# Kernel tuning notes

Measured on AMD Instinct MI355X. Metric: run time of the kernel, lower is better.

Reference implementation:

```python
import jax, jax.numpy as jnp
import numpy as np
from jax import lax

B, S, D, G, V = 32, 8, 128, 32, 64   # batch, slots, hidden_dim, grid_size, vocab_size
K, ED = 128, 32                       # VQ codebook size, code dim


def _conv(x, w, b, pad):
    # standard Conv2d, NCHW / OIHW
    y = lax.conv_general_dilated(x, w, (1, 1), [(pad, pad), (pad, pad)],
                                 dimension_numbers=('NCHW', 'OIHW', 'NCHW'))
    return y + b[None, :, None, None]


def _convT(x, w, b):
    # ConvTranspose2d(k=5, stride=1, padding=2) == conv with spatially flipped
    # kernel, padding k-1-p = 2, channels swapped (IOHW layout of torch weight).
    y = lax.conv_general_dilated(x, jnp.flip(w, (2, 3)), (1, 1), [(2, 2), (2, 2)],
                                 dimension_numbers=('NCHW', 'IOHW', 'NCHW'))
    return y + b[None, :, None, None]


def _build_grid(h, w):
    ys = jnp.linspace(0.0, 1.0, h)
    xs = jnp.linspace(0.0, 1.0, w)
    gy, gx = jnp.meshgrid(ys, xs, indexing='ij')
    g = jnp.stack([gy, gx], axis=-1)                 # [H,W,2]
    return jnp.concatenate([g, 1.0 - g], axis=-1)    # [H,W,4]


def setup_inputs() -> dict:
    key = jax.random.key(0)
    ks = jax.random.split(key, 20)
    sc = 0.05
    n = lambda k, sh: jax.random.normal(k, sh, jnp.float32) * sc
    return {
        'latent': jax.random.normal(ks[0], (B, S, D), jnp.float32),
        'pos_w': n(ks[1], (D, 4)),            # Linear(4, hidden): [out,in]
        'pos_b': jnp.zeros((D,), jnp.float32),
        'ct1_w': n(ks[2], (D, 64, 5, 5)),     # ConvTranspose2d: [in,out,kH,kW]
        'ct1_b': jnp.zeros((64,), jnp.float32),
        'ct2_w': n(ks[3], (64, 32, 5, 5)),
        'ct2_b': jnp.zeros((32,), jnp.float32),
        'codebook': jax.random.uniform(ks[4], (K, ED), jnp.float32, -1.0 / K, 1.0 / K),
        'c1_w': n(ks[5], (64, 32, 3, 3)),     # Conv2d: [out,in,kH,kW]
        'c1_b': jnp.zeros((64,), jnp.float32),
        'c2_w': n(ks[6], (V, 64, 3, 3)),
        'c2_b': jnp.zeros((V,), jnp.float32),
        'a1_w': n(ks[7], (64, 32, 3, 3)),
        'a1_b': jnp.zeros((64,), jnp.float32),
        'a2_w': n(ks[8], (1, 64, 3, 3)),
        'a2_b': jnp.zeros((1,), jnp.float32),
    }


def _forward(latent, pos_w, pos_b, ct1_w, ct1_b, ct2_w, ct2_b, codebook,
             c1_w, c1_b, c2_w, c2_b, a1_w, a1_b, a2_w, a2_b):
    b, s, d = latent.shape
    # spatial broadcast of slot latents -> [B*S, D, H, W]
    z = jnp.broadcast_to(latent.reshape(b * s, d, 1, 1), (b * s, d, G, G))
    # soft position embedding
    grid = _build_grid(G, G)                                  # [H,W,4]
    pos = (grid @ pos_w.T + pos_b).transpose(2, 0, 1)[None]   # [1,D,H,W]
    z = z + pos
    # ConvTranspose decoder
    h = jax.nn.relu(_convT(z, ct1_w, ct1_b))
    feat = jax.nn.relu(_convT(h, ct2_w, ct2_b))               # [B*S,32,H,W]
    # VQ bottleneck on channel-last features
    fp = feat.transpose(0, 2, 3, 1)                           # [B*S,H,W,32]
    flat = fp.reshape(-1, ED)                                 # [N,32]
    dist = (jnp.sum(flat * flat, axis=1, keepdims=True)
            + jnp.sum(codebook * codebook, axis=1)
            - 2.0 * flat @ codebook.T)                        # [N,K]
    idx = jnp.argmin(dist, axis=1)                            # [N]
    q = codebook[idx].reshape(fp.shape)                       # gather lookup
    e_loss = jnp.mean((lax.stop_gradient(q) - fp) ** 2)
    q_loss = jnp.mean((q - lax.stop_gradient(fp)) ** 2)
    vq_loss = q_loss + 0.25 * e_loss
    q_ste = fp + lax.stop_gradient(q - fp)                    # straight-through
    vq_feat = q_ste.transpose(0, 3, 1, 2)                     # [B*S,32,H,W]
    # heads
    colors = _conv(jax.nn.silu(_conv(vq_feat, c1_w, c1_b, 1)), c2_w, c2_b, 1)
    colors = colors.reshape(b, s, V, G, G)
    alphas = _conv(jax.nn.silu(_conv(feat, a1_w, a1_b, 1)), a2_w, a2_b, 1)
    alphas = alphas.reshape(b, s, 1, G, G)
    alphas_n = jax.nn.softmax(alphas, axis=1)
    recon = jnp.sum(alphas_n * colors, axis=1)                # [B,V,H,W]
    return recon, alphas_n, vq_loss


def reference(latent, pos_w, pos_b, ct1_w, ct1_b, ct2_w, ct2_b, codebook,
              c1_w, c1_b, c2_w, c2_b, a1_w, a1_b, a2_w, a2_b):
    return _forward(latent, pos_w, pos_b, ct1_w, ct1_b, ct2_w, ct2_b, codebook,
                    c1_w, c1_b, c2_w, c2_b, a1_w, a1_b, a2_w, a2_b)
```

## Files before the change

### kernel.cpp

```cpp
#include <hip/hip_runtime.h>
#include <math.h>

#define AOFF 2097152
#define LOFF 2359296

typedef __attribute__((ext_vector_type(8))) short short8;
typedef __attribute__((ext_vector_type(4))) float f32x4;

__device__ __forceinline__ int clsf(int v) { return v < 2 ? v : (v > 29 ? v - 27 : 2); }

__device__ __forceinline__ unsigned int f2bfu(float x) {
    unsigned int u = __float_as_uint(x);
    return (u + 0x7FFFu + ((u >> 16) & 1u)) >> 16;
}
__device__ __forceinline__ unsigned int cvt2(float a, float b) {
    return f2bfu(a) | (f2bfu(b) << 16);
}
__device__ __forceinline__ float bf2f(unsigned short u) {
    return __uint_as_float(((unsigned int)u) << 16);
}

__global__ void w1t_kernel(const float* __restrict__ w1, float* __restrict__ w1t) {
    int idx = blockIdx.x * 256 + threadIdx.x;
    if (idx >= 204800) return;
    int tap = idx % 25, rest = idx / 25;
    w1t[tap * 8192 + rest] = w1[idx];
}

__global__ void tapabc_kernel(const float* __restrict__ pw, const float* __restrict__ pb,
                              const float* __restrict__ w1t, float* __restrict__ tapabc) {
    __shared__ float A3[384];
    int tap = blockIdx.x, t = threadIdx.x;
    if (t < 128) {
        float p0 = pw[t * 4], p1 = pw[t * 4 + 1], p2 = pw[t * 4 + 2], p3 = pw[t * 4 + 3];
        A3[t] = p2 + p3 + pb[t];
        A3[128 + t] = p0 - p2;
        A3[256 + t] = p1 - p3;
    }
    __syncthreads();
    int o = t & 63, comp = t >> 6;
    const float* wp = w1t + tap * 8192 + o;
    const float* a = A3 + comp * 128;
    float s = 0.f;
    for (int i = 0; i < 128; ++i) s = fmaf(wp[i * 64], a[i], s);
    tapabc[(tap * 64 + o) * 3 + comp] = s;
}

__global__ void pfill_kernel(const float* __restrict__ tapabc, const float* __restrict__ b1,
                             float* __restrict__ P2) {
    __shared__ float uv[75];
    int o = blockIdx.x, t = threadIdx.x;
    if (t < 75) {
        int cls = t / 3, comp = t % 3;
        int cy = cls / 5, cx = cls % 5;
        const int klo[5] = {2, 1, 0, 0, 0}, khi[5] = {4, 4, 4, 3, 2};
        const float inv31 = 1.f / 31.f;
        float s = (comp == 0) ? b1[o] : 0.f;
        for (int ky = klo[cy]; ky <= khi[cy]; ++ky)
            for (int kx = klo[cx]; kx <= khi[cx]; ++kx) {
                int tap = (4 - ky) * 5 + (4 - kx);
                const float* tp = &tapabc[(tap * 64 + o) * 3];
                if (comp == 0) s += tp[0] + tp[1] * (ky - 2) * inv31 + tp[2] * (kx - 2) * inv31;
                else if (comp == 1) s += tp[1] * inv31;
                else s += tp[2] * inv31;
            }
        uv[t] = s;
    }
    __syncthreads();
    int y = t >> 5, x = t & 31;
    int cls = clsf(y) * 5 + clsf(x);
    float val = uv[cls * 3] + uv[cls * 3 + 1] * y + uv[cls * 3 + 2] * x;
    P2[((o >> 1) << 11) + (t << 1) + (o & 1)] = val;
}

__global__ void wsum_kernel(const float* __restrict__ w1, float* __restrict__ Wsum) {
    int idx = blockIdx.x * 256 + threadIdx.x;
    if (idx >= 25 * 128 * 64) return;
    int cls = idx >> 13;
    int i = (idx >> 6) & 127;
    int o = idx & 63;
    int cy = cls / 5, cx = cls % 5;
    const int klo[5] = {2, 1, 0, 0, 0}, khi[5] = {4, 4, 4, 3, 2};
    float s = 0.f;
    for (int ky = klo[cy]; ky <= khi[cy]; ++ky)
        for (int kx = klo[cx]; kx <= khi[cx]; ++kx)
            s += w1[(i * 64 + o) * 25 + (4 - ky) * 5 + (4 - kx)];
    Wsum[idx] = s;
}

__global__ void m_kernel(const float* __restrict__ latent, const float* __restrict__ Wsum,
                         float* __restrict__ M) {
    int n = blockIdx.x, cls = blockIdx.y, o = threadIdx.x;
    const float* l = &latent[n * 128];
    const float* w = &Wsum[cls * 8192 + o];
    float a0 = 0.f, a1 = 0.f;
    for (int i = 0; i < 128; i += 2) {
        a0 = fmaf(l[i], w[i * 64], a0);
        a1 = fmaf(l[i + 1], w[(i + 1) * 64], a1);
    }
    M[(n * 25 + cls) * 64 + o] = a0 + a1;
}

__global__ void prep_all_kernel(const float* __restrict__ a1w, const float* __restrict__ c1w,
                                const float* __restrict__ c2w, const float* __restrict__ ct2w,
                                short* __restrict__ wtall) {
    int gid = blockIdx.x * 256 + threadIdx.x;
    if (gid < 36864) {
        const float* src = gid < 18432 ? a1w : c1w;
        int idx = gid < 18432 ? gid : gid - 18432;
        int j = idx & 7, fi = idx >> 3;
        int o = fi % 64, g = (fi / 64) & 3, t = fi / 256;
        int i = g * 8 + j;
        wtall[gid] = (short)f2bfu(src[(o * 32 + i) * 9 + (t / 3) * 3 + (t % 3)]);
    } else if (gid < 73728) {
        int idx = gid - 36864;
        int j = idx & 7, fi = idx >> 3;
        int o = fi % 64, g = (fi / 64) & 3, ks = (fi / 256) & 1, t = fi / 512;
        int i = ks * 32 + g * 8 + j;
        wtall[gid] = (short)f2bfu(c2w[(o * 64 + i) * 9 + (t / 3) * 3 + (t % 3)]);
    } else if (gid < 124928) {
        int idx = gid - 73728;
        int j = idx & 7, fi = idx >> 3;
        int o = fi & 31, g = (fi >> 5) & 3, ks = (fi >> 7) & 1, t = fi >> 8;
        int i = ks * 32 + g * 8 + j;
        int ky = t / 5, kx = t % 5;
        wtall[gid] = (short)f2bfu(ct2w[((i * 32 + o) * 5 + (4 - ky)) * 5 + (4 - kx)]);
    }
}

__global__ __launch_bounds__(256) void conv5_kernel(
        const float* __restrict__ M, const float* __restrict__ P2,
        const short* __restrict__ wt, const float* __restrict__ b2,
        unsigned short* __restrict__ featb) {
    __shared__ __align__(16) short tile[12 * 36 * 40];
    __shared__ float Ml[1600];
    const int n = blockIdx.x, y0 = blockIdx.y * 8;
    const int tid = threadIdx.x, w = tid >> 6, l = tid & 63;
    const int lx = l & 15, lg = l >> 4;

    for (int e = tid; e < 1600; e += 256) Ml[e] = M[n * 1600 + e];
    __syncthreads();

    f32x4 acc[2][2][2];
    #pragma unroll
    for (int m = 0; m < 2; ++m)
        #pragma unroll
        for (int q = 0; q < 2; ++q)
            #pragma unroll
            for (int c = 0; c < 2; ++c) acc[m][q][c] = (f32x4){0.f, 0.f, 0.f, 0.f};

    #pragma unroll 1
    for (int ks = 0; ks < 2; ++ks) {
        if (ks) __syncthreads();
        for (int e = tid; e < 6912; e += 256) {
            int cx = e % 36;
            int q = e / 36;
            int ipl = q & 15;
            int r = q >> 4;
            int gy = y0 - 2 + r, gx = cx - 2;
            unsigned int pack = 0u;
            if (gy >= 0 && gy < 32 && gx >= 0 && gx < 32) {
                int cls = clsf(gy) * 5 + clsf(gx);
                int pp = gy * 32 + gx;
                float2 pv = ((const float2*)P2)[((ks * 16 + ipl) << 10) + pp];
                float2 ml = ((const float2*)Ml)[cls * 32 + ks * 16 + ipl];
                pack = cvt2(fmaxf(ml.x + pv.x, 0.f), fmaxf(ml.y + pv.y, 0.f));
            }
            *(unsigned int*)((char*)tile + (r * 36 + cx) * 80 + ipl * 4) = pack;
        }
        __syncthreads();
        for (int kx = 0; kx < 5; ++kx) {
            short8 af[5][2];
            #pragma unroll
            for (int ky = 0; ky < 5; ++ky)
                #pragma unroll
                for (int m = 0; m < 2; ++m)
                    af[ky][m] = *(const short8*)(wt + (ky * 5 + kx) * 2048 +
                                                 ((ks * 4 + lg) * 32 + m * 16 + lx) * 8);
            #pragma unroll
            for (int colf = 0; colf < 2; ++colf) {
                const int cbase = ((2 * w) * 36 + kx + colf * 16 + lx) * 80 + lg * 16;
                short8 bc[6];
                #pragma unroll
                for (int ir = 0; ir < 6; ++ir)
                    bc[ir] = *(const short8*)((char*)tile + cbase + ir * (36 * 80));
                #pragma unroll
                for (int ky = 0; ky < 5; ++ky)
                    #pragma unroll
                    for (int q = 0; q < 2; ++q)
                        #pragma unroll
                        for (int m = 0; m < 2; ++m)
                            acc[m][q][colf] = __builtin_amdgcn_mfma_f32_16x16x32_bf16(
                                af[ky][m], bc[q + ky], acc[m][q][colf], 0, 0, 0);
            }
        }
    }

    #pragma unroll
    for (int m = 0; m < 2; ++m)
        #pragma unroll
        for (int q = 0; q < 2; ++q)
            #pragma unroll
            for (int colf = 0; colf < 2; ++colf) {
                int yl = 2 * w + q, x = colf * 16 + lx;
                unsigned long long pk = 0ull;
                #pragma unroll
                for (int r = 0; r < 4; ++r) {
                    int och = m * 16 + lg * 4 + r;
                    float v = fmaxf(acc[m][q][colf][r] + b2[och], 0.f);
                    pk |= (unsigned long long)f2bfu(v) << (16 * r);
                }
                *(unsigned long long*)(featb + (n * 1024 + (y0 + yl) * 32 + x) * 32
                                       + m * 16 + lg * 4) = pk;
            }
}

__device__ __forceinline__ void conv3_core(
        const short* __restrict__ tile, const short* __restrict__ wt, int abase,
        f32x4 (&acc)[4][2][2], int w, int lx, int lg) {
    #pragma unroll
    for (int kx = 0; kx < 3; ++kx) {
        short8 af[3][4];
        #pragma unroll
        for (int ky = 0; ky < 3; ++ky)
            #pragma unroll
            for (int m = 0; m < 4; ++m)
                af[ky][m] = *(const short8*)(wt + (ky * 3 + kx) * abase +
                                             (lg * 64 + m * 16 + lx) * 8);
        #pragma unroll
        for (int colf = 0; colf < 2; ++colf) {
            const int cbase = ((2 * w) * 34 + kx + colf * 16 + lx) * 80 + lg * 16;
            short8 bc[4];
            #pragma unroll
            for (int ir = 0; ir < 4; ++ir)
                bc[ir] = *(const short8*)((const char*)tile + cbase + ir * (34 * 80));
            #pragma unroll
            for (int ky = 0; ky < 3; ++ky)
                #pragma unroll
                for (int q = 0; q < 2; ++q)
                    #pragma unroll
                    for (int m = 0; m < 4; ++m)
                        acc[m][q][colf] = __builtin_amdgcn_mfma_f32_16x16x32_bf16(
                            af[ky][m], bc[q + ky], acc[m][q][colf], 0, 0, 0);
        }
    }
}

__device__ __forceinline__ void conv3_epi(
        f32x4 (&acc)[4][2][2], const float* __restrict__ bias,
        unsigned short* __restrict__ out_, int n, int y0, int w, int lx, int lg, int act) {
    #pragma unroll
    for (int m = 0; m < 4; ++m)
        #pragma unroll
        for (int q = 0; q < 2; ++q)
            #pragma unroll
            for (int colf = 0; colf < 2; ++colf) {
                int yl = 2 * w + q, x = colf * 16 + lx;
                unsigned long long pk = 0ull;
                #pragma unroll
                for (int r = 0; r < 4; ++r) {
                    int och = m * 16 + lg * 4 + r;
                    float v = acc[m][q][colf][r] + bias[och];
                    if (act) v = v / (1.f + expf(-v));
                    pk |= (unsigned long long)f2bfu(v) << (16 * r);
                }
                *(unsigned long long*)(out_ + (n * 1024 + (y0 + yl) * 32 + x) * 64
                                       + m * 16 + lg * 4) = pk;
            }
}

template<int ACT>
__global__ __launch_bounds__(256) void conv3d_kernel(
        const unsigned short* __restrict__ in_, const short* __restrict__ wt,
        const float* __restrict__ bias, unsigned short* __restrict__ out_) {
    __shared__ __align__(16) short tileA[10 * 34 * 40];
    __shared__ __align__(16) short tileB[10 * 34 * 40];
    const int n0 = blockIdx.x * 2, y0 = blockIdx.y * 8;
    const int tid = threadIdx.x, w = tid >> 6, l = tid & 63;
    const int lx = l & 15, lg = l >> 4;

    short8 rA[6], rB[6];
    int pxv[6], qcv[6];
    #pragma unroll
    for (int it = 0; it < 6; ++it) {
        int e = tid + it * 256;
        short8 v8 = (short8){0, 0, 0, 0, 0, 0, 0, 0};
        int px = e >> 2, qc = e & 3;
        pxv[it] = px; qcv[it] = qc;
        if (e < 1360) {
            int r = px / 34, cx = px - r * 34;
            int gy = y0 - 1 + r, gx = cx - 1;
            if (gy >= 0 && gy < 32 && gx >= 0 && gx < 32)
                v8 = *(const short8*)(in_ + (n0 * 1024 + gy * 32 + gx) * 32 + qc * 8);
        }
        rA[it] = v8;
    }
    #pragma unroll
    for (int it = 0; it < 6; ++it)
        if (tid + it * 256 < 1360)
            *(short8*)((char*)tileA + pxv[it] * 80 + qcv[it] * 16) = rA[it];
    #pragma unroll
    for (int it = 0; it < 6; ++it) {
        int e = tid + it * 256;
        short8 v8 = (short8){0, 0, 0, 0, 0, 0, 0, 0};
        if (e < 1360) {
            int px = pxv[it], qc = qcv[it];
            int r = px / 34, cx = px - r * 34;
            int gy = y0 - 1 + r, gx = cx - 1;
            if (gy >= 0 && gy < 32 && gx >= 0 && gx < 32)
                v8 = *(const short8*)(in_ + ((n0 + 1) * 1024 + gy * 32 + gx) * 32 + qc * 8);
        }
        rB[it] = v8;
    }
    __syncthreads();

    f32x4 acc[4][2][2];
    #pragma unroll
    for (int m = 0; m < 4; ++m)
        #pragma unroll
        for (int q = 0; q < 2; ++q)
            #pragma unroll
            for (int c = 0; c < 2; ++c) acc[m][q][c] = (f32x4){0.f, 0.f, 0.f, 0.f};
    conv3_core(tileA, wt, 2048, acc, w, lx, lg);

    #pragma unroll
    for (int it = 0; it < 6; ++it)
        if (tid + it * 256 < 1360)
            *(short8*)((char*)tileB + pxv[it] * 80 + qcv[it] * 16) = rB[it];
    conv3_epi(acc, bias, out_, n0, y0, w, lx, lg, ACT);
    __syncthreads();

    #pragma unroll
    for (int m = 0; m < 4; ++m)
        #pragma unroll
        for (int q = 0; q < 2; ++q)
            #pragma unroll
            for (int c = 0; c < 2; ++c) acc[m][q][c] = (f32x4){0.f, 0.f, 0.f, 0.f};
    conv3_core(tileB, wt, 2048, acc, w, lx, lg);
    conv3_epi(acc, bias, out_, n0 + 1, y0, w, lx, lg, ACT);
}

__global__ __launch_bounds__(256) void c2_kernel(
        const unsigned short* __restrict__ in_, const short* __restrict__ wt,
        const float* __restrict__ bias, unsigned short* __restrict__ out_) {
    __shared__ __align__(16) short smem[10 * 34 * 40];
    const int n = blockIdx.x, y0 = blockIdx.y * 8;
    const int tid = threadIdx.x, w = tid >> 6, l = tid & 63;
    const int lx = l & 15, lg = l >> 4;

    short8 r0[6], r1[6];
    int pxv[6], qcv[6];
    #pragma unroll
    for (int it = 0; it < 6; ++it) {
        int e = tid + it * 256;
        int px = e >> 2, qc = e & 3;
        pxv[it] = px; qcv[it] = qc;
        short8 v0 = (short8){0, 0, 0, 0, 0, 0, 0, 0};
        short8 v1 = v0;
        if (e < 1360) {
            int r = px / 34, cx = px - r * 34;
            int gy = y0 - 1 + r, gx = cx - 1;
            if (gy >= 0 && gy < 32 && gx >= 0 && gx < 32) {
                const unsigned short* p = in_ + (n * 1024 + gy * 32 + gx) * 64 + qc * 8;
                v0 = *(const short8*)p;
                v1 = *(const short8*)(p + 32);
            }
        }
        r0[it] = v0; r1[it] = v1;
    }
    #pragma unroll
    for (int it = 0; it < 6; ++it)
        if (tid + it * 256 < 1360)
            *(short8*)((char*)smem + pxv[it] * 80 + qcv[it] * 16) = r0[it];
    __syncthreads();

    f32x4 acc[4][2][2];
    #pragma unroll
    for (int m = 0; m < 4; ++m)
        #pragma unroll
        for (int q = 0; q < 2; ++q)
            #pragma unroll
            for (int c = 0; c < 2; ++c) acc[m][q][c] = (f32x4){0.f, 0.f, 0.f, 0.f};

    #pragma unroll
    for (int kx = 0; kx < 3; ++kx) {
        short8 af[3][4];
        #pragma unroll
        for (int ky = 0; ky < 3; ++ky)
            #pragma unroll
            for (int m = 0; m < 4; ++m)
                af[ky][m] = *(const short8*)(wt + (ky * 3 + kx) * 4096 +
                                             ((0 * 4 + lg) * 64 + m * 16 + lx) * 8);
        #pragma unroll
        for (int colf = 0; colf < 2; ++colf) {
            const int cbase = ((2 * w) * 34 + kx + colf * 16 + lx) * 80 + lg * 16;
            short8 bc[4];
            #pragma unroll
            for (int ir = 0; ir < 4; ++ir)
                bc[ir] = *(const short8*)((char*)smem + cbase + ir * (34 * 80));
            #pragma unroll
            for (int ky = 0; ky < 3; ++ky)
                #pragma unroll
                for (int q = 0; q < 2; ++q)
                    #pragma unroll
                    for (int m = 0; m < 4; ++m)
                        acc[m][q][colf] = __builtin_amdgcn_mfma_f32_16x16x32_bf16(
                            af[ky][m], bc[q + ky], acc[m][q][colf], 0, 0, 0);
        }
    }
    __syncthreads();
    #pragma unroll
    for (int it = 0; it < 6; ++it)
        if (tid + it * 256 < 1360)
            *(short8*)((char*)smem + pxv[it] * 80 + qcv[it] * 16) = r1[it];
    __syncthreads();
    #pragma unroll
    for (int kx = 0; kx < 3; ++kx) {
        short8 af[3][4];
        #pragma unroll
        for (int ky = 0; ky < 3; ++ky)
            #pragma unroll
            for (int m = 0; m < 4; ++m)
                af[ky][m] = *(const short8*)(wt + (ky * 3 + kx) * 4096 +
                                             ((1 * 4 + lg) * 64 + m * 16 + lx) * 8);
        #pragma unroll
        for (int colf = 0; colf < 2; ++colf) {
            const int cbase = ((2 * w) * 34 + kx + colf * 16 + lx) * 80 + lg * 16;
            short8 bc[4];
            #pragma unroll
            for (int ir = 0; ir < 4; ++ir)
                bc[ir] = *(const short8*)((char*)smem + cbase + ir * (34 * 80));
            #pragma unroll
            for (int ky = 0; ky < 3; ++ky)
                #pragma unroll
                for (int q = 0; q < 2; ++q)
                    #pragma unroll
                    for (int m = 0; m < 4; ++m)
                        acc[m][q][colf] = __builtin_amdgcn_mfma_f32_16x16x32_bf16(
                            af[ky][m], bc[q + ky], acc[m][q][colf], 0, 0, 0);
        }
    }

    #pragma unroll
    for (int m = 0; m < 4; ++m)
        #pragma unroll
        for (int q = 0; q < 2; ++q)
            #pragma unroll
            for (int colf = 0; colf < 2; ++colf) {
                int yl = 2 * w + q, x = colf * 16 + lx;
                unsigned long long pk = 0ull;
                #pragma unroll
                for (int r = 0; r < 4; ++r) {
                    int och = m * 16 + lg * 4 + r;
                    float v = acc[m][q][colf][r] + bias[och];
                    pk |= (unsigned long long)f2bfu(v) << (16 * r);
                }
                *(unsigned long long*)(out_ + (n * 1024 + (y0 + yl) * 32 + x) * 64
                                       + m * 16 + lg * 4) = pk;
            }
}

__global__ void a2dot_kernel(const unsigned short* __restrict__ in, const float* __restrict__ w,
                             float* __restrict__ s9) {
    __shared__ float wl[576];
    int t = threadIdx.x;
    for (int e = t; e < 576; e += 256) wl[e] = w[e];
    __syncthreads();
    int p = blockIdx.x * 256 + t;
    float acc[9];
    #pragma unroll
    for (int k = 0; k < 9; ++k) acc[k] = 0.f;
    const unsigned short* ip = in + (long long)p * 64;
    #pragma unroll
    for (int c8 = 0; c8 < 8; ++c8) {
        short8 v8 = *(const short8*)(ip + c8 * 8);
        #pragma unroll
        for (int j = 0; j < 8; ++j) {
            float v = bf2f((unsigned short)v8[j]);
            #pragma unroll
            for (int k = 0; k < 9; ++k) acc[k] = fmaf(v, wl[(c8 * 8 + j) * 9 + k], acc[k]);
        }
    }
    #pragma unroll
    for (int k = 0; k < 9; ++k) s9[(k << 18) + p] = acc[k];
}

__global__ void a2soft_kernel(const float* __restrict__ s9, const float* __restrict__ b2,
                              float* __restrict__ outp) {
    int idx = blockIdx.x * 256 + threadIdx.x;
    if (idx >= 32 * 1024) return;
    int bb = idx >> 10, yx = idx & 1023;
    int y = yx >> 5, x = yx & 31;
    float v[8];
    float bias = b2[0];
    #pragma unroll
    for (int s = 0; s < 8; ++s) {
        int n = bb * 8 + s;
        float a = bias;
        #pragma unroll
        for (int ky = 0; ky < 3; ++ky) {
            int yy = y + ky - 1;
            if (yy < 0 || yy > 31) continue;
            #pragma unroll
            for (int kx = 0; kx < 3; ++kx) {
                int xx = x + kx - 1;
                if (xx < 0 || xx > 31) continue;
                a += s9[((ky * 3 + kx) << 18) + (n << 10) + yy * 32 + xx];
            }
        }
        v[s] = a;
    }
    float m = -3.4e38f;
    #pragma unroll
    for (int s = 0; s < 8; ++s) m = fmaxf(m, v[s]);
    float sum = 0.f;
    #pragma unroll
    for (int s = 0; s < 8; ++s) { v[s] = expf(v[s] - m); sum += v[s]; }
    float inv = 1.f / sum;
    #pragma unroll
    for (int s = 0; s < 8; ++s) outp[AOFF + ((bb * 8 + s) << 10) + yx] = v[s] * inv;
}

__global__ __launch_bounds__(256) void vq_mfma_kernel(
        const unsigned short* __restrict__ featb, const float* __restrict__ codebook,
        unsigned short* __restrict__ qfeat, float* __restrict__ partial) {
    __shared__ float cbf[4096];
    __shared__ __align__(16) short cbh[4096];
    __shared__ float cn[128];
    __shared__ float red[4];
    const int tid = threadIdx.x;
    const int w = tid >> 6, l = tid & 63;
    const int lx = l & 15, lg = l >> 4;

    for (int e = tid; e < 4096; e += 256) {
        float v = codebook[e];
        cbf[e] = v;
        int code = e >> 5, d = e & 31;
        int off = (code * 32 + d) * 2;
        off ^= (code & 7) << 4;
        *(short*)((char*)cbh + off) = (short)f2bfu(v);
    }
    __syncthreads();
    if (tid < 128) {
        float s = 0.f;
        #pragma unroll
        for (int c = 0; c < 32; ++c) { float v = cbf[tid * 32 + c]; s = fmaf(v, v, s); }
        cn[tid] = s;
    }
    short8 af[8];
    #pragma unroll
    for (int m = 0; m < 8; ++m) {
        int code = m * 16 + lx;
        int off = (code * 32 + lg * 8) * 2;
        off ^= (code & 7) << 4;
        af[m] = *(const short8*)((char*)cbh + off);
    }
    __syncthreads();
    float cnh[8][4];
    #pragma unroll
    for (int m = 0; m < 8; ++m)
        #pragma unroll
        for (int r = 0; r < 4; ++r)
            cnh[m][r] = 0.5f * cn[m * 16 + lg * 4 + r];

    const int n = blockIdx.x >> 2;
    const int yxw = (blockIdx.x & 3) * 256 + w * 64;
    float lloss = 0.f;

    #pragma unroll 1
    for (int pxg = 0; pxg < 4; ++pxg) {
        int yx = yxw + pxg * 16 + lx;
        short8 bbs = *(const short8*)(featb + (n * 1024 + yx) * 32 + lg * 8);
        f32x4 S[8];
        #pragma unroll
        for (int m = 0; m < 8; ++m)
            S[m] = __builtin_amdgcn_mfma_f32_16x16x32_bf16(
                af[m], bbs, (f32x4){0.f, 0.f, 0.f, 0.f}, 0, 0, 0);
        float bestv = -3.4e38f; int besti = 0;
        #pragma unroll
        for (int m = 0; m < 8; ++m)
            #pragma unroll
            for (int r = 0; r < 4; ++r) {
                float v = S[m][r] - cnh[m][r];
                int code = m * 16 + lg * 4 + r;
                if (v > bestv) { bestv = v; besti = code; }
            }
        #pragma unroll
        for (int d = 16; d < 64; d <<= 1) {
            float ov = __shfl_xor(bestv, d);
            int oi = __shfl_xor(besti, d);
            if (ov > bestv || (ov == bestv && oi < besti)) { bestv = ov; besti = oi; }
        }
        int offq = (besti * 32 + lg * 8) * 2;
        offq ^= (besti & 7) << 4;
        short8 qh = *(const short8*)((char*)cbh + offq);
        *(short8*)(qfeat + (n * 1024 + yx) * 32 + lg * 8) = qh;
        const float* qf = &cbf[besti * 32 + lg * 8];
        #pragma unroll
        for (int j = 0; j < 8; ++j) {
            float fv = bf2f((unsigned short)bbs[j]);
            float dd = qf[j] - fv;
            lloss = fmaf(dd, dd, lloss);
        }
    }
    for (int off = 32; off > 0; off >>= 1) lloss += __shfl_down(lloss, off);
    if (l == 0) red[w] = lloss;
    __syncthreads();
    if (tid == 0) partial[blockIdx.x] = (red[0] + red[1]) + (red[2] + red[3]);
}

__global__ __launch_bounds__(256) void recon_kernel(
        const unsigned short* __restrict__ colors, float* __restrict__ outp) {
    const int b = blockIdx.x, y8 = blockIdx.y;
    const int tid = threadIdx.x;
    const int yxl = tid & 127, vh = tid >> 7;
    const int yx = y8 * 128 + yxl;
    float acc[32];
    #pragma unroll
    for (int v = 0; v < 32; ++v) acc[v] = 0.f;
    #pragma unroll 1
    for (int s = 0; s < 8; ++s) {
        float a = outp[AOFF + ((b * 8 + s) << 10) + yx];
        const unsigned short* cp = colors + ((b * 8 + s) * 1024 + yx) * 64 + vh * 32;
        #pragma unroll
        for (int k = 0; k < 4; ++k) {
            short8 v8 = *(const short8*)(cp + k * 8);
            #pragma unroll
            for (int j = 0; j < 8; ++j)
                acc[k * 8 + j] = fmaf(a, bf2f((unsigned short)v8[j]), acc[k * 8 + j]);
        }
    }
    #pragma unroll
    for (int v = 0; v < 32; ++v)
        outp[(b * 64 + vh * 32 + v) * 1024 + yx] = acc[v];
}

__global__ void loss_kernel(const float* __restrict__ partial, float* __restrict__ outp) {
    __shared__ float red[4];
    int t = threadIdx.x;
    float s = 0.f;
    for (int i = t; i < 1024; i += 256) s += partial[i];
    for (int o = 32; o > 0; o >>= 1) s += __shfl_down(s, o);
    if ((t & 63) == 0) red[t >> 6] = s;
    __syncthreads();
    if (t == 0) outp[LOFF] = 1.25f * ((red[0] + red[1]) + (red[2] + red[3])) / 8388608.0f;
}

extern "C" void kernel_launch(void* const* d_in, const int* in_sizes, int n_in,
                              void* d_out, int out_size, void* d_ws, size_t ws_size,
                              hipStream_t stream) {
    const float* latent  = (const float*)d_in[0];
    const float* pos_w   = (const float*)d_in[1];
    const float* pos_b   = (const float*)d_in[2];
    const float* ct1_w   = (const float*)d_in[3];
    const float* ct1_b   = (const float*)d_in[4];
    const float* ct2_w   = (const float*)d_in[5];
    const float* ct2_b   = (const float*)d_in[6];
    const float* codebook= (const float*)d_in[7];
    const float* c1_w    = (const float*)d_in[8];
    const float* c1_b    = (const float*)d_in[9];
    const float* c2_w    = (const float*)d_in[10];
    const float* c2_b    = (const float*)d_in[11];
    const float* a1_w    = (const float*)d_in[12];
    const float* a1_b    = (const float*)d_in[13];
    const float* a2_w    = (const float*)d_in[14];
    const float* a2_b    = (const float*)d_in[15];
    float* out = (float*)d_out;

    float* ws     = (float*)d_ws;
    unsigned short* featb = (unsigned short*)ws;
    float* s9     = ws + 8388608;
    float* tapabc = s9 + 2359296;
    float* P      = tapabc + 4800;
    float* M      = P + 65536;
    float* partial= M + 409600;
    float* w1t    = partial + 1024;
    float* Wsum   = w1t + 204800;
    short* wtall  = (short*)(Wsum + 204800);
    short* wtA    = wtall;
    short* wtC1   = wtall + 18432;
    short* wtC2   = wtall + 36864;
    short* wtT2   = wtall + 73728;
    unsigned short* tmpb    = (unsigned short*)(wtall + 124928);
    unsigned short* qfeatb  = tmpb + 16777216;
    unsigned short* colorsb = qfeatb + 8388608;

    w1t_kernel<<<800, 256, 0, stream>>>(ct1_w, w1t);
    tapabc_kernel<<<25, 192, 0, stream>>>(pos_w, pos_b, w1t, tapabc);
    pfill_kernel<<<64, 1024, 0, stream>>>(tapabc, ct1_b, P);
    wsum_kernel<<<800, 256, 0, stream>>>(ct1_w, Wsum);
    m_kernel<<<dim3(256, 25), 64, 0, stream>>>(latent, Wsum, M);
    prep_all_kernel<<<488, 256, 0, stream>>>(a1_w, c1_w, c2_w, ct2_w, wtall);

    conv5_kernel<<<dim3(256, 4), 256, 0, stream>>>(M, P, wtT2, ct2_b, featb);
    conv3d_kernel<1><<<dim3(128, 4), 256, 0, stream>>>(featb, wtA, a1_b, tmpb);
    a2dot_kernel<<<1024, 256, 0, stream>>>(tmpb, a2_w, s9);
    a2soft_kernel<<<128, 256, 0, stream>>>(s9, a2_b, out);
    vq_mfma_kernel<<<1024, 256, 0, stream>>>(featb, codebook, qfeatb, partial);
    conv3d_kernel<1><<<dim3(128, 4), 256, 0, stream>>>(qfeatb, wtC1, c1_b, tmpb);
    c2_kernel<<<dim3(256, 4), 256, 0, stream>>>(tmpb, wtC2, c2_b, colorsb);
    recon_kernel<<<dim3(32, 8), 256, 0, stream>>>(colorsb, out);
    loss_kernel<<<1, 256, 0, stream>>>(partial, out);
}
```

Measured before the change: 218.0 us.

## Merge independent head stages into heterogeneous kernels sharing one grid

Independent stages now share launches through a blockIdx.y split. The a1 conv and VQ quantization run together in one kernel, and the c1 conv and a2 dot product in a second; the old one-image-at-a-time conv3 replaces the two-image double-buffered tile pipeline. This is meant to cut launch count and fill the GPU better by overlapping unrelated work. The cost is lost overlap of the second image's load with compute, uneven block durations within one grid, and the colors buffer now aliasing the a1 output scratch.

```diff
diff --git a/kernel.cpp b/kernel.cpp
--- a/kernel.cpp
+++ b/kernel.cpp
@@ -215,9 +215,29 @@
             }
 }
 
-__device__ __forceinline__ void conv3_core(
-        const short* __restrict__ tile, const short* __restrict__ wt, int abase,
-        f32x4 (&acc)[4][2][2], int w, int lx, int lg) {
+__device__ __forceinline__ void conv3_img(
+        const unsigned short* __restrict__ in_, const short* __restrict__ wt,
+        const float* __restrict__ bias, unsigned short* __restrict__ out_,
+        short* __restrict__ smem, int n, int y0, int tid, int act) {
+    const int w = tid >> 6, l = tid & 63;
+    const int lx = l & 15, lg = l >> 4;
+    for (int e = tid; e < 1360; e += 256) {
+        int px = e >> 2, qc = e & 3;
+        int r = px / 34, cx = px - r * 34;
+        int gy = y0 - 1 + r, gx = cx - 1;
+        short8 v8 = (short8){0, 0, 0, 0, 0, 0, 0, 0};
+        if (gy >= 0 && gy < 32 && gx >= 0 && gx < 32)
+            v8 = *(const short8*)(in_ + (n * 1024 + gy * 32 + gx) * 32 + qc * 8);
+        *(short8*)((char*)smem + px * 80 + qc * 16) = v8;
+    }
+    __syncthreads();
+    f32x4 acc[4][2][2];
+    #pragma unroll
+    for (int m = 0; m < 4; ++m)
+        #pragma unroll
+        for (int q = 0; q < 2; ++q)
+            #pragma unroll
+            for (int c = 0; c < 2; ++c) acc[m][q][c] = (f32x4){0.f, 0.f, 0.f, 0.f};
     #pragma unroll
     for (int kx = 0; kx < 3; ++kx) {
         short8 af[3][4];
@@ -225,7 +245,7 @@
         for (int ky = 0; ky < 3; ++ky)
             #pragma unroll
             for (int m = 0; m < 4; ++m)
-                af[ky][m] = *(const short8*)(wt + (ky * 3 + kx) * abase +
+                af[ky][m] = *(const short8*)(wt + (ky * 3 + kx) * 2048 +
                                              (lg * 64 + m * 16 + lx) * 8);
         #pragma unroll
         for (int colf = 0; colf < 2; ++colf) {
@@ -233,7 +253,7 @@
             short8 bc[4];
             #pragma unroll
             for (int ir = 0; ir < 4; ++ir)
-                bc[ir] = *(const short8*)((const char*)tile + cbase + ir * (34 * 80));
+                bc[ir] = *(const short8*)((const char*)smem + cbase + ir * (34 * 80));
             #pragma unroll
             for (int ky = 0; ky < 3; ++ky)
                 #pragma unroll
@@ -244,11 +264,6 @@
                             af[ky][m], bc[q + ky], acc[m][q][colf], 0, 0, 0);
         }
     }
-}
-
-__device__ __forceinline__ void conv3_epi(
-        f32x4 (&acc)[4][2][2], const float* __restrict__ bias,
-        unsigned short* __restrict__ out_, int n, int y0, int w, int lx, int lg, int act) {
     #pragma unroll
     for (int m = 0; m < 4; ++m)
         #pragma unroll
@@ -269,75 +284,132 @@
             }
 }
 
-template<int ACT>
-__global__ __launch_bounds__(256) void conv3d_kernel(
-        const unsigned short* __restrict__ in_, const short* __restrict__ wt,
-        const float* __restrict__ bias, unsigned short* __restrict__ out_) {
-    __shared__ __align__(16) short tileA[10 * 34 * 40];
-    __shared__ __align__(16) short tileB[10 * 34 * 40];
-    const int n0 = blockIdx.x * 2, y0 = blockIdx.y * 8;
-    const int tid = threadIdx.x, w = tid >> 6, l = tid & 63;
+__global__ __launch_bounds__(256) void head1_kernel(
+        const unsigned short* __restrict__ featb, const float* __restrict__ codebook,
+        const short* __restrict__ wtA, const float* __restrict__ a1b,
+        unsigned short* __restrict__ a1out, unsigned short* __restrict__ qfeat,
+        float* __restrict__ partial) {
+    __shared__ __align__(16) char smraw[27648];
+    const int tid = threadIdx.x, n = blockIdx.x;
+    if (blockIdx.y < 4) {
+        conv3_img(featb, wtA, a1b, a1out, (short*)smraw, n, blockIdx.y * 8, tid, 1);
+        return;
+    }
+    float* cbf = (float*)smraw;
+    short* cbh = (short*)(smraw + 16384);
+    float* cn  = (float*)(smraw + 24576);
+    float* red = (float*)(smraw + 25088);
+    const int w = tid >> 6, l = tid & 63;
     const int lx = l & 15, lg = l >> 4;
 
-    short8 rA[6], rB[6];
-    int pxv[6], qcv[6];
-    #pragma unroll
-    for (int it = 0; it < 6; ++it) {
-        int e = tid + it * 256;
-        short8 v8 = (short8){0, 0, 0, 0, 0, 0, 0, 0};
-        int px = e >> 2, qc = e & 3;
-        pxv[it] = px; qcv[it] = qc;
-        if (e < 1360) {
-            int r = px / 34, cx = px - r * 34;
-            int gy = y0 - 1 + r, gx = cx - 1;
-            if (gy >= 0 && gy < 32 && gx >= 0 && gx < 32)
-                v8 = *(const short8*)(in_ + (n0 * 1024 + gy * 32 + gx) * 32 + qc * 8);
-        }
-        rA[it] = v8;
-    }
-    #pragma unroll
-    for (int it = 0; it < 6; ++it)
-        if (tid + it * 256 < 1360)
-            *(short8*)((char*)tileA + pxv[it] * 80 + qcv[it] * 16) = rA[it];
-    #pragma unroll
-    for (int it = 0; it < 6; ++it) {
-        int e = tid + it * 256;
-        short8 v8 = (short8){0, 0, 0, 0, 0, 0, 0, 0};
-        if (e < 1360) {
-            int px = pxv[it], qc = qcv[it];
-            int r = px / 34, cx = px - r * 34;
-            int gy = y0 - 1 + r, gx = cx - 1;
-            if (gy >= 0 && gy < 32 && gx >= 0 && gx < 32)
-                v8 = *(const short8*)(in_ + ((n0 + 1) * 1024 + gy * 32 + gx) * 32 + qc * 8);
-        }
-        rB[it] = v8;
-    }
-    __syncthreads();
-
-    f32x4 acc[4][2][2];
-    #pragma unroll
-    for (int m = 0; m < 4; ++m)
-        #pragma unroll
-        for (int q = 0; q < 2; ++q)
-            #pragma unroll
-            for (int c = 0; c < 2; ++c) acc[m][q][c] = (f32x4){0.f, 0.f, 0.f, 0.f};
-    conv3_core(tileA, wt, 2048, acc, w, lx, lg);
-
-    #pragma unroll
-    for (int it = 0; it < 6; ++it)
-        if (tid + it * 256 < 1360)
-            *(short8*)((char*)tileB + pxv[it] * 80 + qcv[it] * 16) = rB[it];
-    conv3_epi(acc, bias, out_, n0, y0, w, lx, lg, ACT);
-    __syncthreads();
-
-    #pragma unroll
-    for (int m = 0; m < 4; ++m)
-        #pragma unroll
-        for (int q = 0; q < 2; ++q)
-            #pragma unroll
-            for (int c = 0; c < 2; ++c) acc[m][q][c] = (f32x4){0.f, 0.f, 0.f, 0.f};
-    conv3_core(tileB, wt, 2048, acc, w, lx, lg);
-    conv3_epi(acc, bias, out_, n0 + 1, y0, w, lx, lg, ACT);
+    for (int e = tid; e < 4096; e += 256) {
+        float v = codebook[e];
+        cbf[e] = v;
+        int code = e >> 5, d = e & 31;
+        int off = (code * 32 + d) * 2;
+        off ^= (code & 7) << 4;
+        *(short*)((char*)cbh + off) = (short)f2bfu(v);
+    }
+    __syncthreads();
+    if (tid < 128) {
+        float s = 0.f;
+        #pragma unroll
+        for (int c = 0; c < 32; ++c) { float v = cbf[tid * 32 + c]; s = fmaf(v, v, s); }
+        cn[tid] = s;
+    }
+    short8 af[8];
+    #pragma unroll
+    for (int m = 0; m < 8; ++m) {
+        int code = m * 16 + lx;
+        int off = (code * 32 + lg * 8) * 2;
+        off ^= (code & 7) << 4;
+        af[m] = *(const short8*)((char*)cbh + off);
+    }
+    __syncthreads();
+    float cnh[8][4];
+    #pragma unroll
+    for (int m = 0; m < 8; ++m)
+        #pragma unroll
+        for (int r = 0; r < 4; ++r)
+            cnh[m][r] = 0.5f * cn[m * 16 + lg * 4 + r];
+
+    float lloss = 0.f;
+    #pragma unroll 1
+    for (int it = 0; it < 16; ++it) {
+        int yx = w * 256 + (it >> 2) * 64 + (it & 3) * 16 + lx;
+        short8 bbs = *(const short8*)(featb + (n * 1024 + yx) * 32 + lg * 8);
+        f32x4 S[8];
+        #pragma unroll
+        for (int m = 0; m < 8; ++m)
+            S[m] = __builtin_amdgcn_mfma_f32_16x16x32_bf16(
+                af[m], bbs, (f32x4){0.f, 0.f, 0.f, 0.f}, 0, 0, 0);
+        float bestv = -3.4e38f; int besti = 0;
+        #pragma unroll
+        for (int m = 0; m < 8; ++m)
+            #pragma unroll
+            for (int r = 0; r < 4; ++r) {
+                float v = S[m][r] - cnh[m][r];
+                int code = m * 16 + lg * 4 + r;
+                if (v > bestv) { bestv = v; besti = code; }
+            }
+        #pragma unroll
+        for (int d = 16; d < 64; d <<= 1) {
+            float ov = __shfl_xor(bestv, d);
+            int oi = __shfl_xor(besti, d);
+            if (ov > bestv || (ov == bestv && oi < besti)) { bestv = ov; besti = oi; }
+        }
+        int offq = (besti * 32 + lg * 8) * 2;
+        offq ^= (besti & 7) << 4;
+        short8 qh = *(const short8*)((char*)cbh + offq);
+        *(short8*)(qfeat + (n * 1024 + yx) * 32 + lg * 8) = qh;
+        const float* qf = &cbf[besti * 32 + lg * 8];
+        #pragma unroll
+        for (int j = 0; j < 8; ++j) {
+            float fv = bf2f((unsigned short)bbs[j]);
+            float dd = qf[j] - fv;
+            lloss = fmaf(dd, dd, lloss);
+        }
+    }
+    for (int off = 32; off > 0; off >>= 1) lloss += __shfl_down(lloss, off);
+    if (l == 0) red[w] = lloss;
+    __syncthreads();
+    if (tid == 0) partial[n] = (red[0] + red[1]) + (red[2] + red[3]);
+}
+
+__global__ __launch_bounds__(256) void head2_kernel(
+        const unsigned short* __restrict__ qfeat, const short* __restrict__ wtC1,
+        const float* __restrict__ c1b, unsigned short* __restrict__ c1out,
+        const unsigned short* __restrict__ a1out, const float* __restrict__ a2w,
+        float* __restrict__ s9) {
+    __shared__ __align__(16) char smraw[27648];
+    const int tid = threadIdx.x, n = blockIdx.x;
+    if (blockIdx.y < 4) {
+        conv3_img(qfeat, wtC1, c1b, c1out, (short*)smraw, n, blockIdx.y * 8, tid, 1);
+        return;
+    }
+    float* wl = (float*)smraw;
+    for (int e = tid; e < 576; e += 256) wl[e] = a2w[e];
+    __syncthreads();
+    #pragma unroll 1
+    for (int pp = 0; pp < 4; ++pp) {
+        int p = (n << 10) + pp * 256 + tid;
+        float acc[9];
+        #pragma unroll
+        for (int k = 0; k < 9; ++k) acc[k] = 0.f;
+        const unsigned short* ip = a1out + (long long)p * 64;
+        #pragma unroll
+        for (int c8 = 0; c8 < 8; ++c8) {
+            short8 v8 = *(const short8*)(ip + c8 * 8);
+            #pragma unroll
+            for (int j = 0; j < 8; ++j) {
+                float v = bf2f((unsigned short)v8[j]);
+                #pragma unroll
+                for (int k = 0; k < 9; ++k) acc[k] = fmaf(v, wl[(c8 * 8 + j) * 9 + k], acc[k]);
+            }
+        }
+        #pragma unroll
+        for (int k = 0; k < 9; ++k) s9[(k << 18) + p] = acc[k];
+    }
 }
 
 __global__ __launch_bounds__(256) void c2_kernel(
@@ -390,7 +462,7 @@
             #pragma unroll
             for (int m = 0; m < 4; ++m)
                 af[ky][m] = *(const short8*)(wt + (ky * 3 + kx) * 4096 +
-                                             ((0 * 4 + lg) * 64 + m * 16 + lx) * 8);
+                                             (lg * 64 + m * 16 + lx) * 8);
         #pragma unroll
         for (int colf = 0; colf < 2; ++colf) {
             const int cbase = ((2 * w) * 34 + kx + colf * 16 + lx) * 80 + lg * 16;
@@ -422,7 +494,7 @@
             #pragma unroll
             for (int m = 0; m < 4; ++m)
                 af[ky][m] = *(const short8*)(wt + (ky * 3 + kx) * 4096 +
-                                             ((1 * 4 + lg) * 64 + m * 16 + lx) * 8);
+                                             ((4 + lg) * 64 + m * 16 + lx) * 8);
         #pragma unroll
         for (int colf = 0; colf < 2; ++colf) {
             const int cbase = ((2 * w) * 34 + kx + colf * 16 + lx) * 80 + lg * 16;
@@ -458,31 +530,6 @@
                 *(unsigned long long*)(out_ + (n * 1024 + (y0 + yl) * 32 + x) * 64
                                        + m * 16 + lg * 4) = pk;
             }
-}
-
-__global__ void a2dot_kernel(const unsigned short* __restrict__ in, const float* __restrict__ w,
-                             float* __restrict__ s9) {
-    __shared__ float wl[576];
-    int t = threadIdx.x;
-    for (int e = t; e < 576; e += 256) wl[e] = w[e];
-    __syncthreads();
-    int p = blockIdx.x * 256 + t;
-    float acc[9];
-    #pragma unroll
-    for (int k = 0; k < 9; ++k) acc[k] = 0.f;
-    const unsigned short* ip = in + (long long)p * 64;
-    #pragma unroll
-    for (int c8 = 0; c8 < 8; ++c8) {
-        short8 v8 = *(const short8*)(ip + c8 * 8);
-        #pragma unroll
-        for (int j = 0; j < 8; ++j) {
-            float v = bf2f((unsigned short)v8[j]);
-            #pragma unroll
-            for (int k = 0; k < 9; ++k) acc[k] = fmaf(v, wl[(c8 * 8 + j) * 9 + k], acc[k]);
-        }
-    }
-    #pragma unroll
-    for (int k = 0; k < 9; ++k) s9[(k << 18) + p] = acc[k];
 }
 
 __global__ void a2soft_kernel(const float* __restrict__ s9, const float* __restrict__ b2,
@@ -521,94 +568,6 @@
     for (int s = 0; s < 8; ++s) outp[AOFF + ((bb * 8 + s) << 10) + yx] = v[s] * inv;
 }
 
-__global__ __launch_bounds__(256) void vq_mfma_kernel(
-        const unsigned short* __restrict__ featb, const float* __restrict__ codebook,
-        unsigned short* __restrict__ qfeat, float* __restrict__ partial) {
-    __shared__ float cbf[4096];
-    __shared__ __align__(16) short cbh[4096];
-    __shared__ float cn[128];
-    __shared__ float red[4];
-    const int tid = threadIdx.x;
-    const int w = tid >> 6, l = tid & 63;
-    const int lx = l & 15, lg = l >> 4;
-
-    for (int e = tid; e < 4096; e += 256) {
-        float v = codebook[e];
-        cbf[e] = v;
-        int code = e >> 5, d = e & 31;
-        int off = (code * 32 + d) * 2;
-        off ^= (code & 7) << 4;
-        *(short*)((char*)cbh + off) = (short)f2bfu(v);
-    }
-    __syncthreads();
-    if (tid < 128) {
-        float s = 0.f;
-        #pragma unroll
-        for (int c = 0; c < 32; ++c) { float v = cbf[tid * 32 + c]; s = fmaf(v, v, s); }
-        cn[tid] = s;
-    }
-    short8 af[8];
-    #pragma unroll
-    for (int m = 0; m < 8; ++m) {
-        int code = m * 16 + lx;
-        int off = (code * 32 + lg * 8) * 2;
-        off ^= (code & 7) << 4;
-        af[m] = *(const short8*)((char*)cbh + off);
-    }
-    __syncthreads();
-    float cnh[8][4];
-    #pragma unroll
-    for (int m = 0; m < 8; ++m)
-        #pragma unroll
-        for (int r = 0; r < 4; ++r)
-            cnh[m][r] = 0.5f * cn[m * 16 + lg * 4 + r];
-
-    const int n = blockIdx.x >> 2;
-    const int yxw = (blockIdx.x & 3) * 256 + w * 64;
-    float lloss = 0.f;
-
-    #pragma unroll 1
-    for (int pxg = 0; pxg < 4; ++pxg) {
-        int yx = yxw + pxg * 16 + lx;
-        short8 bbs = *(const short8*)(featb + (n * 1024 + yx) * 32 + lg * 8);
-        f32x4 S[8];
-        #pragma unroll
-        for (int m = 0; m < 8; ++m)
-            S[m] = __builtin_amdgcn_mfma_f32_16x16x32_bf16(
-                af[m], bbs, (f32x4){0.f, 0.f, 0.f, 0.f}, 0, 0, 0);
-        float bestv = -3.4e38f; int besti = 0;
-        #pragma unroll
-        for (int m = 0; m < 8; ++m)
-            #pragma unroll
-            for (int r = 0; r < 4; ++r) {
-                float v = S[m][r] - cnh[m][r];
-                int code = m * 16 + lg * 4 + r;
-                if (v > bestv) { bestv = v; besti = code; }
-            }
-        #pragma unroll
-        for (int d = 16; d < 64; d <<= 1) {
-            float ov = __shfl_xor(bestv, d);
-            int oi = __shfl_xor(besti, d);
-            if (ov > bestv || (ov == bestv && oi < besti)) { bestv = ov; besti = oi; }
-        }
-        int offq = (besti * 32 + lg * 8) * 2;
-        offq ^= (besti & 7) << 4;
-        short8 qh = *(const short8*)((char*)cbh + offq);
-        *(short8*)(qfeat + (n * 1024 + yx) * 32 + lg * 8) = qh;
-        const float* qf = &cbf[besti * 32 + lg * 8];
-        #pragma unroll
-        for (int j = 0; j < 8; ++j) {
-            float fv = bf2f((unsigned short)bbs[j]);
-            float dd = qf[j] - fv;
-            lloss = fmaf(dd, dd, lloss);
-        }
-    }
-    for (int off = 32; off > 0; off >>= 1) lloss += __shfl_down(lloss, off);
-    if (l == 0) red[w] = lloss;
-    __syncthreads();
-    if (tid == 0) partial[blockIdx.x] = (red[0] + red[1]) + (red[2] + red[3]);
-}
-
 __global__ __launch_bounds__(256) void recon_kernel(
         const unsigned short* __restrict__ colors, float* __restrict__ outp) {
     const int b = blockIdx.x, y8 = blockIdx.y;
@@ -638,8 +597,7 @@
 __global__ void loss_kernel(const float* __restrict__ partial, float* __restrict__ outp) {
     __shared__ float red[4];
     int t = threadIdx.x;
-    float s = 0.f;
-    for (int i = t; i < 1024; i += 256) s += partial[i];
+    float s = (t < 256) ? partial[t] : 0.f;
     for (int o = 32; o > 0; o >>= 1) s += __shfl_down(s, o);
     if ((t & 63) == 0) red[t >> 6] = s;
     __syncthreads();
@@ -683,7 +641,8 @@
     short* wtT2   = wtall + 73728;
     unsigned short* tmpb    = (unsigned short*)(wtall + 124928);
     unsigned short* qfeatb  = tmpb + 16777216;
-    unsigned short* colorsb = qfeatb + 8388608;
+    unsigned short* c1outb  = qfeatb + 8388608;
+    unsigned short* colorsb = tmpb;
 
     w1t_kernel<<<800, 256, 0, stream>>>(ct1_w, w1t);
     tapabc_kernel<<<25, 192, 0, stream>>>(pos_w, pos_b, w1t, tapabc);
@@ -693,12 +652,12 @@
     prep_all_kernel<<<488, 256, 0, stream>>>(a1_w, c1_w, c2_w, ct2_w, wtall);
 
     conv5_kernel<<<dim3(256, 4), 256, 0, stream>>>(M, P, wtT2, ct2_b, featb);
-    conv3d_kernel<1><<<dim3(128, 4), 256, 0, stream>>>(featb, wtA, a1_b, tmpb);
-    a2dot_kernel<<<1024, 256, 0, stream>>>(tmpb, a2_w, s9);
+    head1_kernel<<<dim3(256, 5), 256, 0, stream>>>(
+        featb, codebook, wtA, a1_b, tmpb, qfeatb, partial);
+    head2_kernel<<<dim3(256, 5), 256, 0, stream>>>(
+        qfeatb, wtC1, c1_b, c1outb, tmpb, a2_w, s9);
     a2soft_kernel<<<128, 256, 0, stream>>>(s9, a2_b, out);
-    vq_mfma_kernel<<<1024, 256, 0, stream>>>(featb, codebook, qfeatb, partial);
-    conv3d_kernel<1><<<dim3(128, 4), 256, 0, stream>>>(qfeatb, wtC1, c1_b, tmpb);
-    c2_kernel<<<dim3(256, 4), 256, 0, stream>>>(tmpb, wtC2, c2_b, colorsb);
+    c2_kernel<<<dim3(256, 4), 256, 0, stream>>>(c1outb, wtC2, c2_b, colorsb);
     recon_kernel<<<dim3(32, 8), 256, 0, stream>>>(colorsb, out);
     loss_kernel<<<1, 256, 0, stream>>>(partial, out);
 }
```

New measurement: 226.7 us. 4.0% more time.

## Shrink conv3 blocks to one image and four rows for higher occupancy

Applied to the files above, without the earlier changes.

Replaces the two-image, eight-row-per-block 3x3 conv kernel (with its register-staged double buffer) with a simpler kernel where each block handles one image and four output rows, and each wave one row. The grid grows from 512 to 2048 blocks, shared memory per block shrinks, accumulators halve, and launch bounds request 6 blocks per CU. The aim is to cut register and LDS pressure so more waves overlap global loads with MFMA work. In exchange, halo rows are reloaded more often relative to output and the cross-image load/compute overlap is lost. The c2 kernel index edits are cosmetic.

```diff
diff --git a/kernel.cpp b/kernel.cpp
--- a/kernel.cpp
+++ b/kernel.cpp
@@ -215,129 +215,74 @@
             }
 }
 
-__device__ __forceinline__ void conv3_core(
-        const short* __restrict__ tile, const short* __restrict__ wt, int abase,
-        f32x4 (&acc)[4][2][2], int w, int lx, int lg) {
-    #pragma unroll
-    for (int kx = 0; kx < 3; ++kx) {
-        short8 af[3][4];
-        #pragma unroll
-        for (int ky = 0; ky < 3; ++ky)
-            #pragma unroll
-            for (int m = 0; m < 4; ++m)
-                af[ky][m] = *(const short8*)(wt + (ky * 3 + kx) * abase +
-                                             (lg * 64 + m * 16 + lx) * 8);
-        #pragma unroll
-        for (int colf = 0; colf < 2; ++colf) {
-            const int cbase = ((2 * w) * 34 + kx + colf * 16 + lx) * 80 + lg * 16;
-            short8 bc[4];
-            #pragma unroll
-            for (int ir = 0; ir < 4; ++ir)
-                bc[ir] = *(const short8*)((const char*)tile + cbase + ir * (34 * 80));
-            #pragma unroll
-            for (int ky = 0; ky < 3; ++ky)
-                #pragma unroll
-                for (int q = 0; q < 2; ++q)
-                    #pragma unroll
-                    for (int m = 0; m < 4; ++m)
-                        acc[m][q][colf] = __builtin_amdgcn_mfma_f32_16x16x32_bf16(
-                            af[ky][m], bc[q + ky], acc[m][q][colf], 0, 0, 0);
-        }
-    }
-}
-
-__device__ __forceinline__ void conv3_epi(
-        f32x4 (&acc)[4][2][2], const float* __restrict__ bias,
-        unsigned short* __restrict__ out_, int n, int y0, int w, int lx, int lg, int act) {
-    #pragma unroll
-    for (int m = 0; m < 4; ++m)
-        #pragma unroll
-        for (int q = 0; q < 2; ++q)
-            #pragma unroll
-            for (int colf = 0; colf < 2; ++colf) {
-                int yl = 2 * w + q, x = colf * 16 + lx;
-                unsigned long long pk = 0ull;
-                #pragma unroll
-                for (int r = 0; r < 4; ++r) {
-                    int och = m * 16 + lg * 4 + r;
-                    float v = acc[m][q][colf][r] + bias[och];
-                    if (act) v = v / (1.f + expf(-v));
-                    pk |= (unsigned long long)f2bfu(v) << (16 * r);
-                }
-                *(unsigned long long*)(out_ + (n * 1024 + (y0 + yl) * 32 + x) * 64
-                                       + m * 16 + lg * 4) = pk;
-            }
-}
-
 template<int ACT>
-__global__ __launch_bounds__(256) void conv3d_kernel(
+__global__ __launch_bounds__(256, 6) void conv3_kernel(
         const unsigned short* __restrict__ in_, const short* __restrict__ wt,
         const float* __restrict__ bias, unsigned short* __restrict__ out_) {
-    __shared__ __align__(16) short tileA[10 * 34 * 40];
-    __shared__ __align__(16) short tileB[10 * 34 * 40];
-    const int n0 = blockIdx.x * 2, y0 = blockIdx.y * 8;
+    __shared__ __align__(16) short smem[6 * 34 * 40];
+    const int n = blockIdx.x, y0 = blockIdx.y * 4;
     const int tid = threadIdx.x, w = tid >> 6, l = tid & 63;
     const int lx = l & 15, lg = l >> 4;
 
-    short8 rA[6], rB[6];
-    int pxv[6], qcv[6];
-    #pragma unroll
-    for (int it = 0; it < 6; ++it) {
-        int e = tid + it * 256;
+    for (int e = tid; e < 816; e += 256) {
+        int px = e >> 2, qc = e & 3;
+        int r = px / 34, cx = px - r * 34;
+        int gy = y0 - 1 + r, gx = cx - 1;
         short8 v8 = (short8){0, 0, 0, 0, 0, 0, 0, 0};
-        int px = e >> 2, qc = e & 3;
-        pxv[it] = px; qcv[it] = qc;
-        if (e < 1360) {
-            int r = px / 34, cx = px - r * 34;
-            int gy = y0 - 1 + r, gx = cx - 1;
-            if (gy >= 0 && gy < 32 && gx >= 0 && gx < 32)
-                v8 = *(const short8*)(in_ + (n0 * 1024 + gy * 32 + gx) * 32 + qc * 8);
-        }
-        rA[it] = v8;
-    }
-    #pragma unroll
-    for (int it = 0; it < 6; ++it)
-        if (tid + it * 256 < 1360)
-            *(short8*)((char*)tileA + pxv[it] * 80 + qcv[it] * 16) = rA[it];
-    #pragma unroll
-    for (int it = 0; it < 6; ++it) {
-        int e = tid + it * 256;
-        short8 v8 = (short8){0, 0, 0, 0, 0, 0, 0, 0};
-        if (e < 1360) {
-            int px = pxv[it], qc = qcv[it];
-            int r = px / 34, cx = px - r * 34;
-            int gy = y0 - 1 + r, gx = cx - 1;
-            if (gy >= 0 && gy < 32 && gx >= 0 && gx < 32)
-                v8 = *(const short8*)(in_ + ((n0 + 1) * 1024 + gy * 32 + gx) * 32 + qc * 8);
-        }
-        rB[it] = v8;
-    }
-    __syncthreads();
-
-    f32x4 acc[4][2][2];
+        if (gy >= 0 && gy < 32 && gx >= 0 && gx < 32)
+            v8 = *(const short8*)(in_ + (n * 1024 + gy * 32 + gx) * 32 + qc * 8);
+        *(short8*)((char*)smem + px * 80 + qc * 16) = v8;
+    }
+    __syncthreads();
+
+    f32x4 acc[4][2];
     #pragma unroll
     for (int m = 0; m < 4; ++m)
         #pragma unroll
-        for (int q = 0; q < 2; ++q)
-            #pragma unroll
-            for (int c = 0; c < 2; ++c) acc[m][q][c] = (f32x4){0.f, 0.f, 0.f, 0.f};
-    conv3_core(tileA, wt, 2048, acc, w, lx, lg);
-
-    #pragma unroll
-    for (int it = 0; it < 6; ++it)
-        if (tid + it * 256 < 1360)
-            *(short8*)((char*)tileB + pxv[it] * 80 + qcv[it] * 16) = rB[it];
-    conv3_epi(acc, bias, out_, n0, y0, w, lx, lg, ACT);
-    __syncthreads();
+        for (int c = 0; c < 2; ++c) acc[m][c] = (f32x4){0.f, 0.f, 0.f, 0.f};
+
+    #pragma unroll
+    for (int kx = 0; kx < 3; ++kx) {
+        short8 bc[2][3];
+        #pragma unroll
+        for (int colf = 0; colf < 2; ++colf) {
+            const int cbase = (w * 34 + kx + colf * 16 + lx) * 80 + lg * 16;
+            #pragma unroll
+            for (int ir = 0; ir < 3; ++ir)
+                bc[colf][ir] = *(const short8*)((char*)smem + cbase + ir * (34 * 80));
+        }
+        #pragma unroll
+        for (int m = 0; m < 4; ++m) {
+            short8 af[3];
+            #pragma unroll
+            for (int ky = 0; ky < 3; ++ky)
+                af[ky] = *(const short8*)(wt + (ky * 3 + kx) * 2048 +
+                                          (lg * 64 + m * 16 + lx) * 8);
+            #pragma unroll
+            for (int ky = 0; ky < 3; ++ky)
+                #pragma unroll
+                for (int colf = 0; colf < 2; ++colf)
+                    acc[m][colf] = __builtin_amdgcn_mfma_f32_16x16x32_bf16(
+                        af[ky], bc[colf][ky], acc[m][colf], 0, 0, 0);
+        }
+    }
 
     #pragma unroll
     for (int m = 0; m < 4; ++m)
         #pragma unroll
-        for (int q = 0; q < 2; ++q)
-            #pragma unroll
-            for (int c = 0; c < 2; ++c) acc[m][q][c] = (f32x4){0.f, 0.f, 0.f, 0.f};
-    conv3_core(tileB, wt, 2048, acc, w, lx, lg);
-    conv3_epi(acc, bias, out_, n0 + 1, y0, w, lx, lg, ACT);
+        for (int colf = 0; colf < 2; ++colf) {
+            int x = colf * 16 + lx;
+            unsigned long long pk = 0ull;
+            #pragma unroll
+            for (int r = 0; r < 4; ++r) {
+                int och = m * 16 + lg * 4 + r;
+                float v = acc[m][colf][r] + bias[och];
+                if (ACT == 1) v = v / (1.f + expf(-v));
+                pk |= (unsigned long long)f2bfu(v) << (16 * r);
+            }
+            *(unsigned long long*)(out_ + (n * 1024 + (y0 + w) * 32 + x) * 64
+                                   + m * 16 + lg * 4) = pk;
+        }
 }
 
 __global__ __launch_bounds__(256) void c2_kernel(
@@ -390,7 +335,7 @@
             #pragma unroll
             for (int m = 0; m < 4; ++m)
                 af[ky][m] = *(const short8*)(wt + (ky * 3 + kx) * 4096 +
-                                             ((0 * 4 + lg) * 64 + m * 16 + lx) * 8);
+                                             (lg * 64 + m * 16 + lx) * 8);
         #pragma unroll
         for (int colf = 0; colf < 2; ++colf) {
             const int cbase = ((2 * w) * 34 + kx + colf * 16 + lx) * 80 + lg * 16;
@@ -422,7 +367,7 @@
             #pragma unroll
             for (int m = 0; m < 4; ++m)
                 af[ky][m] = *(const short8*)(wt + (ky * 3 + kx) * 4096 +
-                                             ((1 * 4 + lg) * 64 + m * 16 + lx) * 8);
+                                             ((4 + lg) * 64 + m * 16 + lx) * 8);
         #pragma unroll
         for (int colf = 0; colf < 2; ++colf) {
             const int cbase = ((2 * w) * 34 + kx + colf * 16 + lx) * 80 + lg * 16;
@@ -693,11 +638,11 @@
     prep_all_kernel<<<488, 256, 0, stream>>>(a1_w, c1_w, c2_w, ct2_w, wtall);
 
     conv5_kernel<<<dim3(256, 4), 256, 0, stream>>>(M, P, wtT2, ct2_b, featb);
-    conv3d_kernel<1><<<dim3(128, 4), 256, 0, stream>>>(featb, wtA, a1_b, tmpb);
+    conv3_kernel<1><<<dim3(256, 8), 256, 0, stream>>>(featb, wtA, a1_b, tmpb);
     a2dot_kernel<<<1024, 256, 0, stream>>>(tmpb, a2_w, s9);
     a2soft_kernel<<<128, 256, 0, stream>>>(s9, a2_b, out);
     vq_mfma_kernel<<<1024, 256, 0, stream>>>(featb, codebook, qfeatb, partial);
-    conv3d_kernel<1><<<dim3(128, 4), 256, 0, stream>>>(qfeatb, wtC1, c1_b, tmpb);
+    conv3_kernel<1><<<dim3(256, 8), 256, 0, stream>>>(qfeatb, wtC1, c1_b, tmpb);
     c2_kernel<<<dim3(256, 4), 256, 0, stream>>>(tmpb, wtC2, c2_b, colorsb);
     recon_kernel<<<dim3(32, 8), 256, 0, stream>>>(colorsb, out);
     loss_kernel<<<1, 256, 0, stream>>>(partial, out);
```

Result: slower. 226.2 us (+3.8%).
